# Kernel tuning notes

Measured on AMD Instinct MI355X. Metric: run time of the kernel, lower is better.

## Reference

```python
import jax, jax.numpy as jnp
import numpy as np

START_ID = 0  # vocab.wd_to_id['<START>']

B, T, V = 128, 256, 1000
C = H = E = 512          # context_size == hidden_size (hidden initialized to context)
IN = C + E               # LSTMCell input size


def setup_inputs() -> dict:
    key = jax.random.key(0)
    ks = jax.random.split(key, 10)
    s = 1.0 / np.sqrt(H)
    return {
        "context": jax.random.normal(ks[0], (B, C), dtype=jnp.float32),
        "target_tensor": jax.random.randint(ks[1], (B, T), 0, V),
        "coin": jax.random.uniform(ks[2], (T,), dtype=jnp.float32),
        "embed_table": jax.random.normal(ks[3], (V, E), dtype=jnp.float32) * 0.02,
        "W_ih": jax.random.uniform(ks[4], (4 * H, IN), dtype=jnp.float32, minval=-s, maxval=s),
        "W_hh": jax.random.uniform(ks[5], (4 * H, H), dtype=jnp.float32, minval=-s, maxval=s),
        "b_ih": jax.random.uniform(ks[6], (4 * H,), dtype=jnp.float32, minval=-s, maxval=s),
        "b_hh": jax.random.uniform(ks[7], (4 * H,), dtype=jnp.float32, minval=-s, maxval=s),
        "W_out": jax.random.uniform(ks[8], (V, H), dtype=jnp.float32, minval=-s, maxval=s),
        "b_out": jax.random.uniform(ks[9], (V,), dtype=jnp.float32, minval=-s, maxval=s),
    }


def reference(context, target_tensor, coin, embed_table, W_ih, W_hh, b_ih, b_hh, W_out, b_out):
    Bsz, Csz = context.shape
    Tlen = target_tensor.shape[1]
    Hsz = W_hh.shape[1]
    Vsz = W_out.shape[0]

    # teacher token for step i is target[:, i-1]; step 0 uses START
    prev_tok = jnp.concatenate(
        [jnp.full((Bsz, 1), START_ID, dtype=target_tensor.dtype), target_tensor[:, :-1]],
        axis=1,
    ).T  # (T, B)

    h0 = context                                   # hidden initialized to context
    c0 = jnp.zeros((Bsz, Hsz), dtype=context.dtype)
    logits0 = jnp.zeros((Bsz, Vsz), dtype=context.dtype)
    steps = jnp.arange(Tlen)

    def step(carry, xs):
        h, c, prev_logits = carry
        tok, r, i = xs
        greedy = jnp.argmax(prev_logits, axis=1)               # previous prediction
        idx = jnp.where(r > 0.5, tok, jnp.where(i == 0, START_ID, greedy))
        emb = embed_table[idx]                                 # (B, E)
        x = jnp.concatenate([context, emb], axis=1)            # (B, C+E)
        gates = x @ W_ih.T + b_ih + h @ W_hh.T + b_hh          # (B, 4H)
        ig, fg, gg, og = jnp.split(gates, 4, axis=1)           # torch order i,f,g,o
        c_new = jax.nn.sigmoid(fg) * c + jax.nn.sigmoid(ig) * jnp.tanh(gg)
        h_new = jax.nn.sigmoid(og) * jnp.tanh(c_new)
        logits = h_new @ W_out.T + b_out                       # (B, V)
        return (h_new, c_new, logits), logits

    (h, c, _), outs = jax.lax.scan(step, (h0, c0, logits0), (prev_tok, coin, steps))
    return outs.transpose(1, 0, 2), h, c  # (B, T, V), (B, H), (B, H)
```

## Files before the change

### kernel.cpp

```cpp
#include <hip/hip_runtime.h>
#include <cstdint>
#include <cstddef>

#define B_SZ 128
#define T_SZ 256
#define V_SZ 1000
#define H_SZ 512
#define NG   2048
#define VP   1024

typedef unsigned long long u64;

__device__ __forceinline__ unsigned fkey(float f) {
  unsigned u = __float_as_uint(f);
  return (u & 0x80000000u) ? ~u : (u | 0x80000000u);
}
__device__ __forceinline__ float sigf(float x) { return 1.0f / (1.0f + expf(-x)); }

__device__ __forceinline__ float aload(const float* p) {
  return __hip_atomic_load(p, __ATOMIC_RELAXED, __HIP_MEMORY_SCOPE_AGENT);
}
__device__ __forceinline__ float4 aload4(const float* p) {
  float4 r;
  r.x = __hip_atomic_load(p + 0, __ATOMIC_RELAXED, __HIP_MEMORY_SCOPE_AGENT);
  r.y = __hip_atomic_load(p + 1, __ATOMIC_RELAXED, __HIP_MEMORY_SCOPE_AGENT);
  r.z = __hip_atomic_load(p + 2, __ATOMIC_RELAXED, __HIP_MEMORY_SCOPE_AGENT);
  r.w = __hip_atomic_load(p + 3, __ATOMIC_RELAXED, __HIP_MEMORY_SCOPE_AGENT);
  return r;
}
__device__ __forceinline__ void astore(float* p, float v) {
  __hip_atomic_store(p, v, __ATOMIC_RELAXED, __HIP_MEMORY_SCOPE_AGENT);
}
__device__ __forceinline__ u64 aload64(const u64* p) {
  return __hip_atomic_load(p, __ATOMIC_RELAXED, __HIP_MEMORY_SCOPE_AGENT);
}
__device__ __forceinline__ void astore64(u64* p, u64 v) {
  __hip_atomic_store(p, v, __ATOMIC_RELAXED, __HIP_MEMORY_SCOPE_AGENT);
}

__device__ __forceinline__ void flag_barrier(unsigned* arrive, unsigned gen) {
  __syncthreads();
  if (threadIdx.x == 0)
    __hip_atomic_store(arrive + blockIdx.x, gen, __ATOMIC_RELEASE, __HIP_MEMORY_SCOPE_AGENT);
  if (threadIdx.x < 64) {
    const int base = threadIdx.x * 4;
    for (;;) {
      bool ok = true;
#pragma unroll
      for (int j = 0; j < 4; ++j)
        ok &= (__hip_atomic_load(arrive + base + j, __ATOMIC_RELAXED,
                                 __HIP_MEMORY_SCOPE_AGENT) >= gen);
      if (__all(ok)) break;
      __builtin_amdgcn_s_sleep(2);
    }
  }
  __syncthreads();
}


__global__ void k_transpose(const float* __restrict__ src, int srcLD, int col_off,
                            float* __restrict__ dst, int dstLD, int n_valid) {
  __shared__ float tile[32][33];
  const int tid = threadIdx.x;
  const int k0 = blockIdx.y * 32, n0 = blockIdx.x * 32;
  const int nl = tid >> 3, kq = (tid & 7) * 4;
  float4 v = make_float4(0.f, 0.f, 0.f, 0.f);
  if (n0 + nl < n_valid)
    v = *(const float4*)(src + (size_t)(n0 + nl) * srcLD + col_off + k0 + kq);
  tile[nl][kq + 0] = v.x; tile[nl][kq + 1] = v.y;
  tile[nl][kq + 2] = v.z; tile[nl][kq + 3] = v.w;
  __syncthreads();
  const int kl = tid >> 3, nq = (tid & 7) * 4;
  float4 o;
  o.x = tile[nq + 0][kl]; o.y = tile[nq + 1][kl];
  o.z = tile[nq + 2][kl]; o.w = tile[nq + 3][kl];
  *(float4*)(dst + (size_t)(k0 + kl) * dstLD + n0 + nq) = o;
}

__global__ void k_base(const float* __restrict__ ctx, const float* __restrict__ Wtc,
                       const float* __restrict__ b_ih, const float* __restrict__ b_hh,
                       float* __restrict__ base) {
  const int tid = threadIdx.x;
  const int n0 = blockIdx.x * 32, m0 = blockIdx.y * 32;
  const int ml = tid >> 3, ng = (tid & 7) * 4;
  const float* a = ctx + (size_t)(m0 + ml) * H_SZ;
  const float* b = Wtc + n0 + ng;
  float acc0 = 0.f, acc1 = 0.f, acc2 = 0.f, acc3 = 0.f;
#pragma unroll 4
  for (int k = 0; k < H_SZ; ++k) {
    float av = a[k];
    float4 bv = *(const float4*)(b + (size_t)k * NG);
    acc0 = fmaf(av, bv.x, acc0); acc1 = fmaf(av, bv.y, acc1);
    acc2 = fmaf(av, bv.z, acc2); acc3 = fmaf(av, bv.w, acc3);
  }
  const int n = n0 + ng;
  float* o = base + (size_t)(m0 + ml) * NG + n;
  o[0] = acc0 + b_ih[n + 0] + b_hh[n + 0];
  o[1] = acc1 + b_ih[n + 1] + b_hh[n + 1];
  o[2] = acc2 + b_ih[n + 2] + b_hh[n + 2];
  o[3] = acc3 + b_ih[n + 3] + b_hh[n + 3];
}

__global__ void k_init(const float* __restrict__ ctx, const float* __restrict__ b_out,
                       float* __restrict__ h0, float* __restrict__ bo,
                       unsigned* __restrict__ arrive) {
  const int i = blockIdx.x * 256 + threadIdx.x;
  h0[i] = ctx[i];
  if (i < VP) bo[i] = (i < V_SZ) ? b_out[i] : 0.f;
  if (i < 256) arrive[i] = 0u;
}

__global__ __launch_bounds__(512, 2) void k_persist(
    const float* __restrict__ Wt, const float* __restrict__ WoT,
    const float* __restrict__ base, const float* __restrict__ etbl,
    const float* __restrict__ coin, const int* __restrict__ tgt,
    const float* __restrict__ bo, float* __restrict__ h0buf, float* __restrict__ h1buf,
    float* __restrict__ out, u64* __restrict__ pk, unsigned* __restrict__ arrive) {
  __shared__ float smem[9216];
  __shared__ int idx_s[32];
  const int tid = threadIdx.x;
  const int bid = blockIdx.x;
  const int xcd = bid & 7, slot = bid >> 3;

  const int qt = xcd * 8 + (slot >> 2);
  const int mtA = slot & 3;
  const int q0 = qt * 8, m0A = mtA * 32;
  const int vt = xcd * 4 + (slot & 3);
  const int mtB = slot >> 2;
  const int n0B = vt * 32, m0B = mtB * 16;

  const int w = tid >> 6, lane = tid & 63;
  const int rg = lane >> 3, cg = lane & 7;
  float* As = smem + w * 1152;
  float* Bs = As + 576;
  const int kbA = w * 128;
  const int amA = lane >> 2, afA = (lane & 3) * 4;
  const int bkA = lane >> 3;
  const int bnA = (lane & 7) * 4;
  const int colA = (bnA >> 3) * 512 + q0 + (bnA & 7);
  float* As2 = smem + w * 896;
  float* Bs2 = As2 + 320;
  const int kbB = w * 64;
  const int amB = lane >> 2;

  const int mlc = tid >> 3, qlc = tid & 7;
  float bsr[4];
  size_t hIdx = 0;
  if (tid < 256) {
#pragma unroll
    for (int g = 0; g < 4; ++g)
      bsr[g] = base[(size_t)(m0A + mlc) * NG + g * 512 + q0 + qlc];
    hIdx = (size_t)(m0A + mlc) * H_SZ + q0 + qlc;
  }
  float creg = 0.f;

  const int mlb = tid >> 5, nlb = tid & 31;
  const int ngB = n0B + nlb, mgB = m0B + mlb;
  const float bor = bo[ngB];
  const size_t outBase = (size_t)mgB * ((size_t)T_SZ * V_SZ) + ngB;

  unsigned gen = 0;

#pragma unroll 1
  for (int t = 0; t < T_SZ; ++t) {
    const float* hRead  = (t & 1) ? h1buf : h0buf;
    float*       hWrite = (t & 1) ? h0buf : h1buf;

    if (tid < 32) {
      int id = 0;
      if (t > 0) {
        if (coin[t] > 0.5f) {
          id = tgt[(m0A + tid) * T_SZ + (t - 1)];
        } else {
          const u64* p = pk + (size_t)(m0A + tid) * 32;
          u64 best = 0ull;
#pragma unroll
          for (int q = 0; q < 32; ++q) { u64 v = aload64(p + q); best = (v > best) ? v : best; }
          id = (int)(~(unsigned)best);
        }
      }
      idx_s[tid] = id;
    }
    __syncthreads();

    {
      float acc[4][4];
#pragma unroll
      for (int i = 0; i < 4; ++i)
#pragma unroll
        for (int j = 0; j < 4; ++j) acc[i][j] = 0.f;

      float4 ra[2], rb[2];
      auto loadA = [&](int s, float4* r) {
        const int k = kbA + s * 16 + afA;
#pragma unroll
        for (int i = 0; i < 2; ++i) {
          const int m_ = amA + i * 16;
          if (k < 512)
            r[i] = *(const float4*)(etbl + (size_t)idx_s[m_] * 512 + k);
          else
            r[i] = aload4(hRead + (size_t)(m0A + m_) * H_SZ + (k - 512));
        }
      };
      auto loadB = [&](int s, float4* r) {
#pragma unroll
        for (int i = 0; i < 2; ++i)
          r[i] = *(const float4*)(Wt + (size_t)(kbA + s * 16 + bkA + i * 8) * NG + colA);
      };

      loadA(0, ra); loadB(0, rb);
#pragma unroll 1
      for (int s = 0; s < 8; ++s) {
#pragma unroll
        for (int i = 0; i < 2; ++i) {
          const int m_ = amA + i * 16;
          As[(afA + 0) * 36 + m_] = ra[i].x;
          As[(afA + 1) * 36 + m_] = ra[i].y;
          As[(afA + 2) * 36 + m_] = ra[i].z;
          As[(afA + 3) * 36 + m_] = ra[i].w;
          *(float4*)(Bs + (bkA + i * 8) * 36 + bnA) = rb[i];
        }
        float4 na[2], nb[2];
        if (s < 7) { loadA(s + 1, na); loadB(s + 1, nb); }
#pragma unroll
        for (int k = 0; k < 16; ++k) {
          float4 a = *(const float4*)(As + k * 36 + rg * 4);
          float4 b = *(const float4*)(Bs + k * 36 + cg * 4);
          acc[0][0] = fmaf(a.x, b.x, acc[0][0]); acc[0][1] = fmaf(a.x, b.y, acc[0][1]);
          acc[0][2] = fmaf(a.x, b.z, acc[0][2]); acc[0][3] = fmaf(a.x, b.w, acc[0][3]);
          acc[1][0] = fmaf(a.y, b.x, acc[1][0]); acc[1][1] = fmaf(a.y, b.y, acc[1][1]);
          acc[1][2] = fmaf(a.y, b.z, acc[1][2]); acc[1][3] = fmaf(a.y, b.w, acc[1][3]);
          acc[2][0] = fmaf(a.z, b.x, acc[2][0]); acc[2][1] = fmaf(a.z, b.y, acc[2][1]);
          acc[2][2] = fmaf(a.z, b.z, acc[2][2]); acc[2][3] = fmaf(a.z, b.w, acc[2][3]);
          acc[3][0] = fmaf(a.w, b.x, acc[3][0]); acc[3][1] = fmaf(a.w, b.y, acc[3][1]);
          acc[3][2] = fmaf(a.w, b.z, acc[3][2]); acc[3][3] = fmaf(a.w, b.w, acc[3][3]);
        }
        if (s < 7) { ra[0] = na[0]; ra[1] = na[1]; rb[0] = nb[0]; rb[1] = nb[1]; }
      }
      __syncthreads();
#pragma unroll
      for (int i = 0; i < 4; ++i)
#pragma unroll
        for (int j = 0; j < 4; ++j)
          smem[w * 1024 + (rg * 4 + i) * 32 + cg * 4 + j] = acc[i][j];
      __syncthreads();

      if (tid < 256) {
        float gv[4];
#pragma unroll
        for (int g = 0; g < 4; ++g) {
          float s_ = bsr[g];
          const int j = g * 8 + qlc;
#pragma unroll
          for (int w2 = 0; w2 < 8; ++w2) s_ += smem[w2 * 1024 + mlc * 32 + j];
          gv[g] = s_;
        }
        const float cn = sigf(gv[1]) * creg + sigf(gv[0]) * tanhf(gv[2]);
        creg = cn;
        astore(hWrite + hIdx, sigf(gv[3]) * tanhf(cn));
      }
    }
    flag_barrier(arrive, ++gen);

    {
      float acc[2][4];
#pragma unroll
      for (int i = 0; i < 2; ++i)
#pragma unroll
        for (int j = 0; j < 4; ++j) acc[i][j] = 0.f;

      float4 ra; float4 rb[2];
      auto loadA2 = [&](int s, float4& r) {
        r = aload4(hWrite + (size_t)(m0B + amB) * H_SZ + kbB + s * 16 + afA);
      };
      auto loadB2 = [&](int s, float4* r) {
#pragma unroll
        for (int i = 0; i < 2; ++i)
          r[i] = *(const float4*)(WoT + (size_t)(kbB + s * 16 + bkA + i * 8) * VP + n0B + bnA);
      };

      loadA2(0, ra); loadB2(0, rb);
#pragma unroll 1
      for (int s = 0; s < 4; ++s) {
        As2[(afA + 0) * 20 + amB] = ra.x;
        As2[(afA + 1) * 20 + amB] = ra.y;
        As2[(afA + 2) * 20 + amB] = ra.z;
        As2[(afA + 3) * 20 + amB] = ra.w;
#pragma unroll
        for (int i = 0; i < 2; ++i) *(float4*)(Bs2 + (bkA + i * 8) * 36 + bnA) = rb[i];
        float4 na; float4 nb[2];
        if (s < 3) { loadA2(s + 1, na); loadB2(s + 1, nb); }
#pragma unroll
        for (int k = 0; k < 16; ++k) {
          float2 a = *(const float2*)(As2 + k * 20 + rg * 2);
          float4 b = *(const float4*)(Bs2 + k * 36 + cg * 4);
          acc[0][0] = fmaf(a.x, b.x, acc[0][0]); acc[0][1] = fmaf(a.x, b.y, acc[0][1]);
          acc[0][2] = fmaf(a.x, b.z, acc[0][2]); acc[0][3] = fmaf(a.x, b.w, acc[0][3]);
          acc[1][0] = fmaf(a.y, b.x, acc[1][0]); acc[1][1] = fmaf(a.y, b.y, acc[1][1]);
          acc[1][2] = fmaf(a.y, b.z, acc[1][2]); acc[1][3] = fmaf(a.y, b.w, acc[1][3]);
        }
        if (s < 3) { ra = na; rb[0] = nb[0]; rb[1] = nb[1]; }
      }
      __syncthreads();
#pragma unroll
      for (int i = 0; i < 2; ++i)
#pragma unroll
        for (int j = 0; j < 4; ++j)
          smem[w * 512 + (rg * 2 + i) * 32 + cg * 4 + j] = acc[i][j];
      __syncthreads();

      float sres = bor;
#pragma unroll
      for (int w2 = 0; w2 < 8; ++w2) sres += smem[w2 * 512 + tid];
      u64 p = 0ull;
      if (ngB < V_SZ) {
        out[outBase + (size_t)t * V_SZ] = sres;
        p = ((u64)fkey(sres) << 32) | (u64)(unsigned)(~(unsigned)ngB);
      }
#pragma unroll
      for (int d = 16; d >= 1; d >>= 1) {
        u64 o = __shfl_xor(p, d, 64);
        p = (o > p) ? o : p;
      }
      if (nlb == 0) astore64(pk + (size_t)mgB * 32 + vt, p);
    }
    const bool need_pk_bar = (t + 1 < T_SZ) && !(coin[t + 1] > 0.5f);
    if (need_pk_bar) flag_barrier(arrive, ++gen);
  }

  const size_t off = (size_t)B_SZ * T_SZ * V_SZ;
  if (tid < 256) {
    out[off + (size_t)bid * 256 + tid] = aload(h0buf + (size_t)bid * 256 + tid);
    out[off + 65536 + hIdx] = creg;
  }
}

extern "C" void kernel_launch(void* const* d_in, const int* in_sizes, int n_in,
                              void* d_out, int out_size, void* d_ws, size_t ws_size,
                              hipStream_t stream) {
  (void)in_sizes; (void)n_in; (void)out_size; (void)ws_size;
  const float* ctx   = (const float*)d_in[0];
  const int*   tgt   = (const int*)d_in[1];
  const float* coin  = (const float*)d_in[2];
  const float* etbl  = (const float*)d_in[3];
  const float* W_ih  = (const float*)d_in[4];
  const float* W_hh  = (const float*)d_in[5];
  const float* b_ih  = (const float*)d_in[6];
  const float* b_hh  = (const float*)d_in[7];
  const float* W_out = (const float*)d_in[8];
  const float* b_out = (const float*)d_in[9];
  float* out = (float*)d_out;

  float* ws    = (float*)d_ws;
  float* Wt    = ws;
  float* Wtc   = Wt + 2097152;
  float* WoT   = Wtc + 1048576;
  float* base  = WoT + 524288;
  float* h0    = base + 262144;
  float* h1    = h0 + 65536;
  u64*   pk    = (u64*)(h1 + 65536);
  float* bo    = (float*)(pk + 4096);
  unsigned* arrive = (unsigned*)(bo + 1024);

  hipLaunchKernelGGL(k_transpose, dim3(64, 16), dim3(256), 0, stream,
                     W_ih, 1024, 512, Wt, NG, 2048);
  hipLaunchKernelGGL(k_transpose, dim3(64, 16), dim3(256), 0, stream,
                     W_hh, 512, 0, Wt + (size_t)512 * NG, NG, 2048);
  hipLaunchKernelGGL(k_transpose, dim3(64, 16), dim3(256), 0, stream,
                     W_ih, 1024, 0, Wtc, NG, 2048);
  hipLaunchKernelGGL(k_transpose, dim3(32, 16), dim3(256), 0, stream,
                     W_out, 512, 0, WoT, VP, 1000);
  hipLaunchKernelGGL(k_base, dim3(64, 4), dim3(256), 0, stream, ctx, Wtc, b_ih, b_hh, base);
  hipLaunchKernelGGL(k_init, dim3(256), dim3(256), 0, stream, ctx, b_out, h0, bo, arrive);

  void* args[] = { (void*)&Wt, (void*)&WoT, (void*)&base, (void*)&etbl, (void*)&coin,
                   (void*)&tgt, (void*)&bo, (void*)&h0, (void*)&h1, (void*)&out,
                   (void*)&pk, (void*)&arrive };
  hipLaunchCooperativeKernel((void*)k_persist, dim3(256), dim3(512), args, 0, stream);
}
```

Measured before the change: 12.03 ms.

## Replace all-to-all flag barrier with master broadcast and tagged argmax slots

The grid barrier changes from every block polling all 256 arrival flags to a scheme where block 0 gathers the arrivals and publishes one broadcast flag that the other blocks spin on. The second per-step barrier before the greedy argmax is removed. Each packed argmax slot now carries a step tag in its low byte, and readers spin until the tag matches, which gives point-to-point sync in place of a global one. This is meant to cut global barrier latency in the sequential loop. The arrival store drops from release to relaxed ordering, which risks the h writes not being visible to other blocks on time.

```diff
diff --git a/kernel.cpp b/kernel.cpp
--- a/kernel.cpp
+++ b/kernel.cpp
@@ -38,11 +38,11 @@
   __hip_atomic_store(p, v, __ATOMIC_RELAXED, __HIP_MEMORY_SCOPE_AGENT);
 }
 
-__device__ __forceinline__ void flag_barrier(unsigned* arrive, unsigned gen) {
+__device__ __forceinline__ void bcast_barrier(unsigned* arrive, unsigned gen) {
   __syncthreads();
   if (threadIdx.x == 0)
-    __hip_atomic_store(arrive + blockIdx.x, gen, __ATOMIC_RELEASE, __HIP_MEMORY_SCOPE_AGENT);
-  if (threadIdx.x < 64) {
+    __hip_atomic_store(arrive + blockIdx.x, gen, __ATOMIC_RELAXED, __HIP_MEMORY_SCOPE_AGENT);
+  if (blockIdx.x == 0 && threadIdx.x < 64) {
     const int base = threadIdx.x * 4;
     for (;;) {
       bool ok = true;
@@ -53,6 +53,13 @@
       if (__all(ok)) break;
       __builtin_amdgcn_s_sleep(2);
     }
+    if (threadIdx.x == 0)
+      __hip_atomic_store(arrive + 320, gen, __ATOMIC_RELAXED, __HIP_MEMORY_SCOPE_AGENT);
+  }
+  if (threadIdx.x == 0) {
+    while (__hip_atomic_load(arrive + 320, __ATOMIC_RELAXED,
+                             __HIP_MEMORY_SCOPE_AGENT) < gen)
+      __builtin_amdgcn_s_sleep(2);
   }
   __syncthreads();
 }
@@ -107,7 +114,7 @@
   const int i = blockIdx.x * 256 + threadIdx.x;
   h0[i] = ctx[i];
   if (i < VP) bo[i] = (i < V_SZ) ? b_out[i] : 0.f;
-  if (i < 256) arrive[i] = 0u;
+  if (i < 512) arrive[i] = 0u;
 }
 
 __global__ __launch_bounds__(512, 2) void k_persist(
@@ -159,8 +166,6 @@
   const float bor = bo[ngB];
   const size_t outBase = (size_t)mgB * ((size_t)T_SZ * V_SZ) + ngB;
 
-  unsigned gen = 0;
-
 #pragma unroll 1
   for (int t = 0; t < T_SZ; ++t) {
     const float* hRead  = (t & 1) ? h1buf : h0buf;
@@ -173,10 +178,18 @@
           id = tgt[(m0A + tid) * T_SZ + (t - 1)];
         } else {
           const u64* p = pk + (size_t)(m0A + tid) * 32;
+          const unsigned tagw = (unsigned)((t - 1) & 0xFF);
           u64 best = 0ull;
-#pragma unroll
-          for (int q = 0; q < 32; ++q) { u64 v = aload64(p + q); best = (v > best) ? v : best; }
-          id = (int)(~(unsigned)best);
+#pragma unroll 1
+          for (int q = 0; q < 32; ++q) {
+            u64 v = aload64(p + q);
+            while ((unsigned)(v & 0xFFu) != tagw) {
+              __builtin_amdgcn_s_sleep(1);
+              v = aload64(p + q);
+            }
+            best = (v > best) ? v : best;
+          }
+          id = 1023 - (int)((best >> 8) & 0x3FF);
         }
       }
       idx_s[tid] = id;
@@ -260,7 +273,7 @@
         astore(hWrite + hIdx, sigf(gv[3]) * tanhf(cn));
       }
     }
-    flag_barrier(arrive, ++gen);
+    bcast_barrier(arrive, (unsigned)(t + 1));
 
     {
       float acc[2][4];
@@ -315,7 +328,8 @@
       u64 p = 0ull;
       if (ngB < V_SZ) {
         out[outBase + (size_t)t * V_SZ] = sres;
-        p = ((u64)fkey(sres) << 32) | (u64)(unsigned)(~(unsigned)ngB);
+        p = ((u64)fkey(sres) << 32) | ((u64)(unsigned)(1023 - ngB) << 8)
+            | (u64)(unsigned)(t & 0xFF);
       }
 #pragma unroll
       for (int d = 16; d >= 1; d >>= 1) {
@@ -324,8 +338,6 @@
       }
       if (nlb == 0) astore64(pk + (size_t)mgB * 32 + vt, p);
     }
-    const bool need_pk_bar = (t + 1 < T_SZ) && !(coin[t + 1] > 0.5f);
-    if (need_pk_bar) flag_barrier(arrive, ++gen);
   }
 
   const size_t off = (size_t)B_SZ * T_SZ * V_SZ;
```

After: 10.26 ms. -14.7%, faster.
